# Optimization experiments

Hardware: AMD Instinct MI355X
Metric: run time of the kernel (lower is better)

The kernel has to match this reference:

```python
import jax, jax.numpy as jnp
import numpy as np

N_HEADS = 16


def setup_inputs() -> dict:
    key = jax.random.key(0)
    k1, k2, k3 = jax.random.split(key, 3)
    B, T, D = 2, 2048, 1024
    x = jax.random.normal(k1, (B, T, D), dtype=jnp.float32)
    w_qkv = jax.random.normal(k2, (3 * D, D), dtype=jnp.float32) * 0.02
    w_proj = jax.random.normal(k3, (D, D), dtype=jnp.float32) * (0.02 / np.sqrt(24.0))
    return {"x": x, "w_qkv": w_qkv, "w_proj": w_proj}


def reference(x, w_qkv, w_proj):
    B, T, D = x.shape
    H = N_HEADS
    dh = D // H
    # qkv linear (no bias): x @ w_qkv.T -> [B, T, 3D]
    qkv = jnp.einsum('btd,ed->bte', x, w_qkv)
    q, k, v = jnp.split(qkv, 3, axis=-1)
    q = q.reshape(B, T, H, dh)
    k = k.reshape(B, T, H, dh)
    v = v.reshape(B, T, H, dh)
    # attention with materialized scores [B, H, T, S]
    scores = jnp.einsum('bthd,bshd->bhts', q, k) / jnp.sqrt(jnp.asarray(dh, x.dtype))
    attn = jax.nn.softmax(scores.astype(jnp.float32), axis=-1).astype(x.dtype)
    out = jnp.einsum('bhts,bshd->bthd', attn, v).reshape(B, T, D)
    # output projection (no bias)
    return jnp.einsum('btd,ed->bte', out, w_proj)
```

## Files before the change

kernel.cpp:

```cpp
#include <hip/hip_runtime.h>


typedef __attribute__((ext_vector_type(8))) short s8v;
typedef __attribute__((ext_vector_type(4))) short s4v;
typedef __attribute__((ext_vector_type(8))) unsigned short us8;
typedef __attribute__((ext_vector_type(4))) float f4v;

__device__ __forceinline__ unsigned short f2b(float f) {
    unsigned u = __builtin_bit_cast(unsigned, f);
    u += 0x7FFFu + ((u >> 16) & 1u);
    return (unsigned short)(u >> 16);
}

#if __has_builtin(__builtin_amdgcn_exp2f)
#define EXP2F(x) __builtin_amdgcn_exp2f(x)
#else
#define EXP2F(x) exp2f(x)
#endif

__global__ __launch_bounds__(256) void cvt_all(const float* __restrict__ x,
                                               const float* __restrict__ wq,
                                               const float* __restrict__ wp,
                                               unsigned short* __restrict__ xb,
                                               unsigned short* __restrict__ wqb,
                                               unsigned short* __restrict__ wpb) {
    const int nx = 4096 * 1024 / 4, nq = 3072 * 1024 / 4;
    int i = blockIdx.x * 256 + threadIdx.x;
    const float* s;
    unsigned short* d;
    int j;
    if (i < nx)           { s = x;  d = xb;  j = i; }
    else if (i < nx + nq) { s = wq; d = wqb; j = i - nx; }
    else                  { s = wp; d = wpb; j = i - nx - nq; }
    float4 v = ((const float4*)s)[j];
    ushort4 o;
    o.x = f2b(v.x); o.y = f2b(v.y); o.z = f2b(v.z); o.w = f2b(v.w);
    ((ushort4*)d)[j] = o;
}

#define GLD_LDS16(g, l)                                                                        \
    __builtin_amdgcn_global_load_lds((const __attribute__((address_space(1))) unsigned*)(g),   \
                                     (__attribute__((address_space(3))) unsigned*)(l), 16, 0, 0)

template <bool BF16OUT>
__global__ __launch_bounds__(256) void gemm_nt_bf16(const unsigned short* __restrict__ A,
                                                    const unsigned short* __restrict__ B,
                                                    void* __restrict__ Cv,
                                                    int M, int N, int K) {
    __shared__ unsigned short As[128][32];
    __shared__ unsigned short Bs[128][32];

    const int tid = threadIdx.x;
    const int l = tid & 63, w = tid >> 6;
    const int quad = l >> 4, ln = l & 15;
    const int m0 = blockIdx.y * 128, n0 = blockIdx.x * 128;
    const int wm = (w >> 1) * 64, wn = (w & 1) * 64;

    const f4v fz = {0.f, 0.f, 0.f, 0.f};
    f4v acc[4][4];
#pragma unroll
    for (int i = 0; i < 4; ++i)
#pragma unroll
        for (int j = 0; j < 4; ++j) acc[i][j] = fz;

    const int row0 = tid >> 2, kc = tid & 3;
    for (int k0 = 0; k0 < K; k0 += 32) {
        GLD_LDS16(A + (size_t)(m0 + row0) * K + k0 + kc * 8, &As[row0][kc * 8]);
        GLD_LDS16(B + (size_t)(n0 + row0) * K + k0 + kc * 8, &Bs[row0][kc * 8]);
        GLD_LDS16(A + (size_t)(m0 + row0 + 64) * K + k0 + kc * 8, &As[row0 + 64][kc * 8]);
        GLD_LDS16(B + (size_t)(n0 + row0 + 64) * K + k0 + kc * 8, &Bs[row0 + 64][kc * 8]);
        __syncthreads();

        s8v af[4], bf[4];
#pragma unroll
        for (int mt = 0; mt < 4; ++mt) af[mt] = *(const s8v*)&As[wm + mt * 16 + ln][quad * 8];
#pragma unroll
        for (int nt = 0; nt < 4; ++nt) bf[nt] = *(const s8v*)&Bs[wn + nt * 16 + ln][quad * 8];
#pragma unroll
        for (int mt = 0; mt < 4; ++mt)
#pragma unroll
            for (int nt = 0; nt < 4; ++nt)
                acc[mt][nt] = __builtin_amdgcn_mfma_f32_16x16x32_bf16(af[mt], bf[nt], acc[mt][nt], 0, 0, 0);
        __syncthreads();
    }

#pragma unroll
    for (int mt = 0; mt < 4; ++mt)
#pragma unroll
        for (int nt = 0; nt < 4; ++nt) {
            const size_t row = (size_t)(m0 + wm + mt * 16 + quad * 4);
            const int col = n0 + wn + nt * 16 + ln;
            if (BF16OUT) {
                unsigned short* C = (unsigned short*)Cv;
#pragma unroll
                for (int r = 0; r < 4; ++r) C[(row + r) * N + col] = f2b(acc[mt][nt][r]);
            } else {
                float* C = (float*)Cv;
#pragma unroll
                for (int r = 0; r < 4; ++r) C[(row + r) * N + col] = acc[mt][nt][r];
            }
        }
}

__global__ __launch_bounds__(256) void vtrans(const unsigned short* __restrict__ qkvb,
                                              unsigned short* __restrict__ vtb) {
    __shared__ unsigned Ls[64][65];
    const int tid = threadIdx.x;
    const int t0 = blockIdx.x * 64, h = blockIdx.y, b = blockIdx.z;
#pragma unroll
    for (int it = 0; it < 2; ++it) {
        int idx = tid + it * 256;
        int r = idx >> 3, c8 = idx & 7;
        us8 v = *(const us8*)(qkvb + ((size_t)b * 2048 + t0 + r) * 3072 + 2048 + h * 64 + c8 * 8);
#pragma unroll
        for (int j = 0; j < 8; ++j) Ls[r][c8 * 8 + j] = v[j];
    }
    __syncthreads();
#pragma unroll
    for (int it = 0; it < 2; ++it) {
        int idx = tid + it * 256;
        int d = idx >> 3, tc = idx & 7;
        us8 o;
#pragma unroll
        for (int j = 0; j < 8; ++j) o[j] = (unsigned short)Ls[tc * 8 + j][d];
        *(us8*)(vtb + ((size_t)(b * 16 + h) * 64 + d) * 2048 + t0 + tc * 8) = o;
    }
}

__global__ __launch_bounds__(256) void attn_mfma(const unsigned short* __restrict__ qkvb,
                                                 const unsigned short* __restrict__ vtb,
                                                 unsigned short* __restrict__ attnb) {
    __shared__ unsigned short Qs[64][72];
    __shared__ unsigned short Ks[64][72];
    __shared__ unsigned short Vt[64][72];
    __shared__ unsigned short Ps[64][76];

    const int tid = threadIdx.x;
    const int l = tid & 63, w = tid >> 6;
    const int quad = l >> 4, ln = l & 15;
    const int qb = w * 16;
    const int t0 = blockIdx.x * 64;
    const int h = blockIdx.y, b = blockIdx.z;
    const size_t rowbase = (size_t)b * 2048;
    const unsigned short* Vg = vtb + (size_t)(b * 16 + h) * 64 * 2048;

    const int r0 = tid >> 3,         c0 = (tid & 7) * 8;
    const int r1 = (tid + 256) >> 3, c1 = c0;

    *(us8*)&Qs[r0][c0] = *(const us8*)(qkvb + (rowbase + t0 + r0) * 3072 + h * 64 + c0);
    *(us8*)&Qs[r1][c1] = *(const us8*)(qkvb + (rowbase + t0 + r1) * 3072 + h * 64 + c1);

    const f4v fz = {0.f, 0.f, 0.f, 0.f};
    f4v oacc[4];
#pragma unroll
    for (int i = 0; i < 4; ++i) oacc[i] = fz;
    float lsum[4] = {0.f, 0.f, 0.f, 0.f};

    us8 kreg0 = *(const us8*)(qkvb + (rowbase + r0) * 3072 + 1024 + h * 64 + c0);
    us8 kreg1 = *(const us8*)(qkvb + (rowbase + r1) * 3072 + 1024 + h * 64 + c1);
    us8 vreg0 = *(const us8*)(Vg + (size_t)r0 * 2048 + c0);
    us8 vreg1 = *(const us8*)(Vg + (size_t)r1 * 2048 + c1);

    const float C = 0.18033688011112042f;

    for (int s0 = 0; s0 < 2048; s0 += 64) {
        __syncthreads();
        *(us8*)&Ks[r0][c0] = kreg0;
        *(us8*)&Ks[r1][c1] = kreg1;
        *(us8*)&Vt[r0][c0] = vreg0;
        *(us8*)&Vt[r1][c1] = vreg1;
        __syncthreads();

        if (s0 + 64 < 2048) {
            const int sn = s0 + 64;
            kreg0 = *(const us8*)(qkvb + (rowbase + sn + r0) * 3072 + 1024 + h * 64 + c0);
            kreg1 = *(const us8*)(qkvb + (rowbase + sn + r1) * 3072 + 1024 + h * 64 + c1);
            vreg0 = *(const us8*)(Vg + (size_t)r0 * 2048 + sn + c0);
            vreg1 = *(const us8*)(Vg + (size_t)r1 * 2048 + sn + c1);
        }

        f4v sacc[4];
#pragma unroll
        for (int i = 0; i < 4; ++i) sacc[i] = fz;
#pragma unroll
        for (int ks = 0; ks < 2; ++ks) {
            s8v af = *(const s8v*)&Qs[qb + ln][ks * 32 + quad * 8];
#pragma unroll
            for (int nt = 0; nt < 4; ++nt) {
                s8v bf = *(const s8v*)&Ks[nt * 16 + ln][ks * 32 + quad * 8];
                sacc[nt] = __builtin_amdgcn_mfma_f32_16x16x32_bf16(af, bf, sacc[nt], 0, 0, 0);
            }
        }

#pragma unroll
        for (int nt = 0; nt < 4; ++nt)
#pragma unroll
            for (int r = 0; r < 4; ++r) {
                float p = EXP2F(sacc[nt][r] * C);
                lsum[r] += p;
                Ps[qb + quad * 4 + r][nt * 16 + ln] = f2b(p);
            }

#pragma unroll
        for (int ks = 0; ks < 2; ++ks) {
            s4v plo = *(const s4v*)&Ps[qb + ln][ks * 32 + quad * 8];
            s4v phi = *(const s4v*)&Ps[qb + ln][ks * 32 + quad * 8 + 4];
            s8v pf = __builtin_shufflevector(plo, phi, 0, 1, 2, 3, 4, 5, 6, 7);
#pragma unroll
            for (int nt = 0; nt < 4; ++nt) {
                s8v vf = *(const s8v*)&Vt[nt * 16 + ln][ks * 32 + quad * 8];
                oacc[nt] = __builtin_amdgcn_mfma_f32_16x16x32_bf16(pf, vf, oacc[nt], 0, 0, 0);
            }
        }
    }

    float inv[4];
#pragma unroll
    for (int r = 0; r < 4; ++r) {
        float v = lsum[r];
        v += __shfl_xor(v, 1, 64);
        v += __shfl_xor(v, 2, 64);
        v += __shfl_xor(v, 4, 64);
        v += __shfl_xor(v, 8, 64);
        inv[r] = 1.0f / v;
    }

#pragma unroll
    for (int nt = 0; nt < 4; ++nt)
#pragma unroll
        for (int r = 0; r < 4; ++r) {
            float o = oacc[nt][r] * inv[r];
            attnb[(rowbase + t0 + qb + quad * 4 + r) * 1024 + h * 64 + nt * 16 + ln] = f2b(o);
        }
}

extern "C" void kernel_launch(void* const* d_in, const int* in_sizes, int n_in,
                              void* d_out, int out_size, void* d_ws, size_t ws_size,
                              hipStream_t stream) {
    const float* x      = (const float*)d_in[0];
    const float* w_qkv  = (const float*)d_in[1];
    const float* w_proj = (const float*)d_in[2];
    float* out = (float*)d_out;

    char* p = (char*)d_ws;
    unsigned short* xb    = (unsigned short*)p;  p += (size_t)4096 * 1024 * 2;
    unsigned short* wqb   = (unsigned short*)p;  p += (size_t)3072 * 1024 * 2;
    unsigned short* wpb   = (unsigned short*)p;  p += (size_t)1024 * 1024 * 2;
    unsigned short* qkvb  = (unsigned short*)p;  p += (size_t)4096 * 3072 * 2;
    unsigned short* vtb   = (unsigned short*)p;  p += (size_t)2 * 16 * 64 * 2048 * 2;
    unsigned short* attnb = (unsigned short*)p;  p += (size_t)4096 * 1024 * 2;

    cvt_all<<<8192, 256, 0, stream>>>(x, w_qkv, w_proj, xb, wqb, wpb);

    gemm_nt_bf16<true><<<dim3(3072 / 128, 4096 / 128), 256, 0, stream>>>(xb, wqb, qkvb, 4096, 3072, 1024);

    vtrans<<<dim3(32, 16, 2), 256, 0, stream>>>(qkvb, vtb);

    attn_mfma<<<dim3(32, 16, 2), 256, 0, stream>>>(qkvb, vtb, attnb);

    gemm_nt_bf16<false><<<dim3(1024 / 128, 4096 / 128), 256, 0, stream>>>(attnb, wpb, out, 4096, 1024, 1024);
}
```

Baseline: 215.0 us.

## Fuse V transpose and Q scaling into QKV GEMM, use 32x32 MFMA attention

The QKV GEMM epilogue now writes Q pre-scaled by the softmax constant, writes K into a compact buffer, and writes V already transposed, so the separate vtrans kernel is gone. The attention kernel handles 128 query rows per block with 32x32x16 MFMAs, writes P with packed bf16 stores, and reduces row sums through LDS. The output projection uses a 128x64 tile to launch more blocks for the narrow N=1024 GEMM. Risks are scattered strided stores for the transposed V in the epilogue, higher register and LDS use in attention, and bf16 rounding of the scaled Q.

```diff
diff --git a/kernel.cpp b/kernel.cpp
--- a/kernel.cpp
+++ b/kernel.cpp
@@ -2,14 +2,21 @@
 
 
 typedef __attribute__((ext_vector_type(8))) short s8v;
-typedef __attribute__((ext_vector_type(4))) short s4v;
 typedef __attribute__((ext_vector_type(8))) unsigned short us8;
 typedef __attribute__((ext_vector_type(4))) float f4v;
+typedef __attribute__((ext_vector_type(16))) float f16v;
 
 __device__ __forceinline__ unsigned short f2b(float f) {
     unsigned u = __builtin_bit_cast(unsigned, f);
     u += 0x7FFFu + ((u >> 16) & 1u);
     return (unsigned short)(u >> 16);
+}
+__device__ __forceinline__ unsigned pack2(float a, float b) {
+    unsigned ua = __builtin_bit_cast(unsigned, a);
+    ua += 0x7FFFu + ((ua >> 16) & 1u);
+    unsigned ub = __builtin_bit_cast(unsigned, b);
+    ub += 0x7FFFu + ((ub >> 16) & 1u);
+    return (ua >> 16) | (ub & 0xFFFF0000u);
 }
 
 #if __has_builtin(__builtin_amdgcn_exp2f)
@@ -17,6 +24,8 @@
 #else
 #define EXP2F(x) exp2f(x)
 #endif
+
+#define QSCALE 0.18033688011112042f
 
 __global__ __launch_bounds__(256) void cvt_all(const float* __restrict__ x,
                                                const float* __restrict__ wq,
@@ -42,14 +51,12 @@
     __builtin_amdgcn_global_load_lds((const __attribute__((address_space(1))) unsigned*)(g),   \
                                      (__attribute__((address_space(3))) unsigned*)(l), 16, 0, 0)
 
-template <bool BF16OUT>
-__global__ __launch_bounds__(256) void gemm_nt_bf16(const unsigned short* __restrict__ A,
-                                                    const unsigned short* __restrict__ B,
-                                                    void* __restrict__ Cv,
-                                                    int M, int N, int K) {
+__global__ __launch_bounds__(256) void gemm_qkv(const unsigned short* __restrict__ A,
+                                                const unsigned short* __restrict__ B,
+                                                unsigned short* __restrict__ qkb,
+                                                unsigned short* __restrict__ vtb) {
     __shared__ unsigned short As[128][32];
     __shared__ unsigned short Bs[128][32];
-
     const int tid = threadIdx.x;
     const int l = tid & 63, w = tid >> 6;
     const int quad = l >> 4, ln = l & 15;
@@ -64,13 +71,12 @@
         for (int j = 0; j < 4; ++j) acc[i][j] = fz;
 
     const int row0 = tid >> 2, kc = tid & 3;
-    for (int k0 = 0; k0 < K; k0 += 32) {
-        GLD_LDS16(A + (size_t)(m0 + row0) * K + k0 + kc * 8, &As[row0][kc * 8]);
-        GLD_LDS16(B + (size_t)(n0 + row0) * K + k0 + kc * 8, &Bs[row0][kc * 8]);
-        GLD_LDS16(A + (size_t)(m0 + row0 + 64) * K + k0 + kc * 8, &As[row0 + 64][kc * 8]);
-        GLD_LDS16(B + (size_t)(n0 + row0 + 64) * K + k0 + kc * 8, &Bs[row0 + 64][kc * 8]);
-        __syncthreads();
-
+    for (int k0 = 0; k0 < 1024; k0 += 32) {
+        GLD_LDS16(A + (size_t)(m0 + row0) * 1024 + k0 + kc * 8, &As[row0][kc * 8]);
+        GLD_LDS16(B + (size_t)(n0 + row0) * 1024 + k0 + kc * 8, &Bs[row0][kc * 8]);
+        GLD_LDS16(A + (size_t)(m0 + row0 + 64) * 1024 + k0 + kc * 8, &As[row0 + 64][kc * 8]);
+        GLD_LDS16(B + (size_t)(n0 + row0 + 64) * 1024 + k0 + kc * 8, &Bs[row0 + 64][kc * 8]);
+        __syncthreads();
         s8v af[4], bf[4];
 #pragma unroll
         for (int mt = 0; mt < 4; ++mt) af[mt] = *(const s8v*)&As[wm + mt * 16 + ln][quad * 8];
@@ -88,150 +94,185 @@
     for (int mt = 0; mt < 4; ++mt)
 #pragma unroll
         for (int nt = 0; nt < 4; ++nt) {
-            const size_t row = (size_t)(m0 + wm + mt * 16 + quad * 4);
             const int col = n0 + wn + nt * 16 + ln;
-            if (BF16OUT) {
-                unsigned short* C = (unsigned short*)Cv;
-#pragma unroll
-                for (int r = 0; r < 4; ++r) C[(row + r) * N + col] = f2b(acc[mt][nt][r]);
+            const int row = m0 + wm + mt * 16 + quad * 4;
+            f4v a = acc[mt][nt];
+            if (col < 2048) {
+                const float sc = (col < 1024) ? QSCALE : 1.0f;
+#pragma unroll
+                for (int r = 0; r < 4; ++r)
+                    qkb[(size_t)(row + r) * 2048 + col] = f2b(a[r] * sc);
             } else {
-                float* C = (float*)Cv;
-#pragma unroll
-                for (int r = 0; r < 4; ++r) C[(row + r) * N + col] = acc[mt][nt][r];
-            }
-        }
-}
-
-__global__ __launch_bounds__(256) void vtrans(const unsigned short* __restrict__ qkvb,
-                                              unsigned short* __restrict__ vtb) {
-    __shared__ unsigned Ls[64][65];
-    const int tid = threadIdx.x;
-    const int t0 = blockIdx.x * 64, h = blockIdx.y, b = blockIdx.z;
-#pragma unroll
-    for (int it = 0; it < 2; ++it) {
-        int idx = tid + it * 256;
-        int r = idx >> 3, c8 = idx & 7;
-        us8 v = *(const us8*)(qkvb + ((size_t)b * 2048 + t0 + r) * 3072 + 2048 + h * 64 + c8 * 8);
-#pragma unroll
-        for (int j = 0; j < 8; ++j) Ls[r][c8 * 8 + j] = v[j];
-    }
-    __syncthreads();
-#pragma unroll
-    for (int it = 0; it < 2; ++it) {
-        int idx = tid + it * 256;
-        int d = idx >> 3, tc = idx & 7;
-        us8 o;
-#pragma unroll
-        for (int j = 0; j < 8; ++j) o[j] = (unsigned short)Ls[tc * 8 + j][d];
-        *(us8*)(vtb + ((size_t)(b * 16 + h) * 64 + d) * 2048 + t0 + tc * 8) = o;
-    }
-}
-
-__global__ __launch_bounds__(256) void attn_mfma(const unsigned short* __restrict__ qkvb,
-                                                 const unsigned short* __restrict__ vtb,
-                                                 unsigned short* __restrict__ attnb) {
-    __shared__ unsigned short Qs[64][72];
-    __shared__ unsigned short Ks[64][72];
-    __shared__ unsigned short Vt[64][72];
-    __shared__ unsigned short Ps[64][76];
-
+                const int vd = col - 2048, hh = vd >> 6, dd = vd & 63;
+                const int bb = row >> 11, t = row & 2047;
+                uint2 pk;
+                pk.x = pack2(a[0], a[1]);
+                pk.y = pack2(a[2], a[3]);
+                *(uint2*)&vtb[((size_t)(bb * 16 + hh) * 64 + dd) * 2048 + t] = pk;
+            }
+        }
+}
+
+__global__ __launch_bounds__(256) void gemm_proj(const unsigned short* __restrict__ A,
+                                                 const unsigned short* __restrict__ B,
+                                                 float* __restrict__ C) {
+    __shared__ unsigned short As[128][32];
+    __shared__ unsigned short Bs[64][32];
     const int tid = threadIdx.x;
     const int l = tid & 63, w = tid >> 6;
     const int quad = l >> 4, ln = l & 15;
-    const int qb = w * 16;
-    const int t0 = blockIdx.x * 64;
-    const int h = blockIdx.y, b = blockIdx.z;
-    const size_t rowbase = (size_t)b * 2048;
-    const unsigned short* Vg = vtb + (size_t)(b * 16 + h) * 64 * 2048;
-
-    const int r0 = tid >> 3,         c0 = (tid & 7) * 8;
-    const int r1 = (tid + 256) >> 3, c1 = c0;
-
-    *(us8*)&Qs[r0][c0] = *(const us8*)(qkvb + (rowbase + t0 + r0) * 3072 + h * 64 + c0);
-    *(us8*)&Qs[r1][c1] = *(const us8*)(qkvb + (rowbase + t0 + r1) * 3072 + h * 64 + c1);
+    const int m0 = blockIdx.y * 128, n0 = blockIdx.x * 64;
+    const int wm = w * 32;
 
     const f4v fz = {0.f, 0.f, 0.f, 0.f};
-    f4v oacc[4];
-#pragma unroll
-    for (int i = 0; i < 4; ++i) oacc[i] = fz;
-    float lsum[4] = {0.f, 0.f, 0.f, 0.f};
-
-    us8 kreg0 = *(const us8*)(qkvb + (rowbase + r0) * 3072 + 1024 + h * 64 + c0);
-    us8 kreg1 = *(const us8*)(qkvb + (rowbase + r1) * 3072 + 1024 + h * 64 + c1);
+    f4v acc[2][4];
+#pragma unroll
+    for (int i = 0; i < 2; ++i)
+#pragma unroll
+        for (int j = 0; j < 4; ++j) acc[i][j] = fz;
+
+    const int row0 = tid >> 2, kc = tid & 3;
+    for (int k0 = 0; k0 < 1024; k0 += 32) {
+        GLD_LDS16(A + (size_t)(m0 + row0) * 1024 + k0 + kc * 8, &As[row0][kc * 8]);
+        GLD_LDS16(A + (size_t)(m0 + row0 + 64) * 1024 + k0 + kc * 8, &As[row0 + 64][kc * 8]);
+        GLD_LDS16(B + (size_t)(n0 + row0) * 1024 + k0 + kc * 8, &Bs[row0][kc * 8]);
+        __syncthreads();
+        s8v af[2], bf[4];
+#pragma unroll
+        for (int mt = 0; mt < 2; ++mt) af[mt] = *(const s8v*)&As[wm + mt * 16 + ln][quad * 8];
+#pragma unroll
+        for (int nt = 0; nt < 4; ++nt) bf[nt] = *(const s8v*)&Bs[nt * 16 + ln][quad * 8];
+#pragma unroll
+        for (int mt = 0; mt < 2; ++mt)
+#pragma unroll
+            for (int nt = 0; nt < 4; ++nt)
+                acc[mt][nt] = __builtin_amdgcn_mfma_f32_16x16x32_bf16(af[mt], bf[nt], acc[mt][nt], 0, 0, 0);
+        __syncthreads();
+    }
+
+#pragma unroll
+    for (int mt = 0; mt < 2; ++mt)
+#pragma unroll
+        for (int nt = 0; nt < 4; ++nt) {
+            const int row = m0 + wm + mt * 16 + quad * 4;
+            const int col = n0 + nt * 16 + ln;
+#pragma unroll
+            for (int r = 0; r < 4; ++r) C[(size_t)(row + r) * 1024 + col] = acc[mt][nt][r];
+        }
+}
+
+__global__ __launch_bounds__(256) void attn_mfma(const unsigned short* __restrict__ qkb,
+                                                 const unsigned short* __restrict__ vtb,
+                                                 unsigned short* __restrict__ attnb) {
+    __shared__ unsigned short Qs[128][76];
+    __shared__ unsigned short Ks[64][76];
+    __shared__ unsigned short Vt[64][76];
+    __shared__ unsigned short Ps[128][76];
+    __shared__ float lred[128];
+
+    const int tid = threadIdx.x;
+    const int l = tid & 63, w = tid >> 6;
+    const int m31 = l & 31, h2 = l >> 5;
+    const int qw = w * 32;
+    const int t0 = blockIdx.x * 128;
+    const int hh = blockIdx.y, bb = blockIdx.z;
+    const size_t rowbase = (size_t)bb * 2048;
+    const unsigned short* Vg = vtb + (size_t)(bb * 16 + hh) * 64 * 2048;
+
+#pragma unroll
+    for (int it = 0; it < 4; ++it) {
+        const int idx = tid + it * 256;
+        const int qr = idx >> 3, qc = (idx & 7) * 8;
+        *(us8*)&Qs[qr][qc] = *(const us8*)(qkb + (rowbase + t0 + qr) * 2048 + hh * 64 + qc);
+    }
+
+    const int r0 = tid >> 3, c0 = (tid & 7) * 8;
+
+    f16v zz;
+#pragma unroll
+    for (int i = 0; i < 16; ++i) zz[i] = 0.f;
+    f16v oacc[2];
+    oacc[0] = zz; oacc[1] = zz;
+    float lsum = 0.f;
+
+    us8 kreg0 = *(const us8*)(qkb + (rowbase + r0) * 2048 + 1024 + hh * 64 + c0);
+    us8 kreg1 = *(const us8*)(qkb + (rowbase + r0 + 32) * 2048 + 1024 + hh * 64 + c0);
     us8 vreg0 = *(const us8*)(Vg + (size_t)r0 * 2048 + c0);
-    us8 vreg1 = *(const us8*)(Vg + (size_t)r1 * 2048 + c1);
-
-    const float C = 0.18033688011112042f;
+    us8 vreg1 = *(const us8*)(Vg + (size_t)(r0 + 32) * 2048 + c0);
 
     for (int s0 = 0; s0 < 2048; s0 += 64) {
         __syncthreads();
         *(us8*)&Ks[r0][c0] = kreg0;
-        *(us8*)&Ks[r1][c1] = kreg1;
+        *(us8*)&Ks[r0 + 32][c0] = kreg1;
         *(us8*)&Vt[r0][c0] = vreg0;
-        *(us8*)&Vt[r1][c1] = vreg1;
+        *(us8*)&Vt[r0 + 32][c0] = vreg1;
         __syncthreads();
 
         if (s0 + 64 < 2048) {
             const int sn = s0 + 64;
-            kreg0 = *(const us8*)(qkvb + (rowbase + sn + r0) * 3072 + 1024 + h * 64 + c0);
-            kreg1 = *(const us8*)(qkvb + (rowbase + sn + r1) * 3072 + 1024 + h * 64 + c1);
+            kreg0 = *(const us8*)(qkb + (rowbase + sn + r0) * 2048 + 1024 + hh * 64 + c0);
+            kreg1 = *(const us8*)(qkb + (rowbase + sn + r0 + 32) * 2048 + 1024 + hh * 64 + c0);
             vreg0 = *(const us8*)(Vg + (size_t)r0 * 2048 + sn + c0);
-            vreg1 = *(const us8*)(Vg + (size_t)r1 * 2048 + sn + c1);
-        }
-
-        f4v sacc[4];
-#pragma unroll
-        for (int i = 0; i < 4; ++i) sacc[i] = fz;
-#pragma unroll
-        for (int ks = 0; ks < 2; ++ks) {
-            s8v af = *(const s8v*)&Qs[qb + ln][ks * 32 + quad * 8];
-#pragma unroll
-            for (int nt = 0; nt < 4; ++nt) {
-                s8v bf = *(const s8v*)&Ks[nt * 16 + ln][ks * 32 + quad * 8];
-                sacc[nt] = __builtin_amdgcn_mfma_f32_16x16x32_bf16(af, bf, sacc[nt], 0, 0, 0);
-            }
-        }
-
-#pragma unroll
-        for (int nt = 0; nt < 4; ++nt)
+            vreg1 = *(const us8*)(Vg + (size_t)(r0 + 32) * 2048 + sn + c0);
+        }
+
+        f16v sacc[2];
+        sacc[0] = zz; sacc[1] = zz;
+#pragma unroll
+        for (int k4 = 0; k4 < 4; ++k4) {
+            s8v qf = *(const s8v*)&Qs[qw + m31][k4 * 16 + h2 * 8];
+#pragma unroll
+            for (int st = 0; st < 2; ++st) {
+                s8v kf = *(const s8v*)&Ks[st * 32 + m31][k4 * 16 + h2 * 8];
+                sacc[st] = __builtin_amdgcn_mfma_f32_32x32x16_bf16(kf, qf, sacc[st], 0, 0, 0);
+            }
+        }
+
+#pragma unroll
+        for (int st = 0; st < 2; ++st)
+#pragma unroll
+            for (int g = 0; g < 4; ++g) {
+                float p0 = EXP2F(sacc[st][g * 4 + 0]);
+                float p1 = EXP2F(sacc[st][g * 4 + 1]);
+                float p2 = EXP2F(sacc[st][g * 4 + 2]);
+                float p3 = EXP2F(sacc[st][g * 4 + 3]);
+                lsum += (p0 + p1) + (p2 + p3);
+                uint2 pk;
+                pk.x = pack2(p0, p1);
+                pk.y = pack2(p2, p3);
+                *(uint2*)&Ps[qw + m31][st * 32 + g * 8 + h2 * 4] = pk;
+            }
+
+#pragma unroll
+        for (int k2 = 0; k2 < 4; ++k2) {
+            s8v pf = *(const s8v*)&Ps[qw + m31][k2 * 16 + h2 * 8];
+#pragma unroll
+            for (int nt = 0; nt < 2; ++nt) {
+                s8v vf = *(const s8v*)&Vt[nt * 32 + m31][k2 * 16 + h2 * 8];
+                oacc[nt] = __builtin_amdgcn_mfma_f32_32x32x16_bf16(pf, vf, oacc[nt], 0, 0, 0);
+            }
+        }
+    }
+
+    lsum += __shfl_xor(lsum, 32, 64);
+    lred[qw + m31] = lsum;
+    float inv[16];
+#pragma unroll
+    for (int g = 0; g < 4; ++g)
+#pragma unroll
+        for (int r = 0; r < 4; ++r)
+            inv[g * 4 + r] = 1.0f / lred[qw + 8 * g + 4 * h2 + r];
+
+#pragma unroll
+    for (int nt = 0; nt < 2; ++nt)
+#pragma unroll
+        for (int g = 0; g < 4; ++g)
 #pragma unroll
             for (int r = 0; r < 4; ++r) {
-                float p = EXP2F(sacc[nt][r] * C);
-                lsum[r] += p;
-                Ps[qb + quad * 4 + r][nt * 16 + ln] = f2b(p);
-            }
-
-#pragma unroll
-        for (int ks = 0; ks < 2; ++ks) {
-            s4v plo = *(const s4v*)&Ps[qb + ln][ks * 32 + quad * 8];
-            s4v phi = *(const s4v*)&Ps[qb + ln][ks * 32 + quad * 8 + 4];
-            s8v pf = __builtin_shufflevector(plo, phi, 0, 1, 2, 3, 4, 5, 6, 7);
-#pragma unroll
-            for (int nt = 0; nt < 4; ++nt) {
-                s8v vf = *(const s8v*)&Vt[nt * 16 + ln][ks * 32 + quad * 8];
-                oacc[nt] = __builtin_amdgcn_mfma_f32_16x16x32_bf16(pf, vf, oacc[nt], 0, 0, 0);
-            }
-        }
-    }
-
-    float inv[4];
-#pragma unroll
-    for (int r = 0; r < 4; ++r) {
-        float v = lsum[r];
-        v += __shfl_xor(v, 1, 64);
-        v += __shfl_xor(v, 2, 64);
-        v += __shfl_xor(v, 4, 64);
-        v += __shfl_xor(v, 8, 64);
-        inv[r] = 1.0f / v;
-    }
-
-#pragma unroll
-    for (int nt = 0; nt < 4; ++nt)
-#pragma unroll
-        for (int r = 0; r < 4; ++r) {
-            float o = oacc[nt][r] * inv[r];
-            attnb[(rowbase + t0 + qb + quad * 4 + r) * 1024 + h * 64 + nt * 16 + ln] = f2b(o);
-        }
+                const int qrow = 8 * g + 4 * h2 + r;
+                float o = oacc[nt][g * 4 + r] * inv[g * 4 + r];
+                attnb[(rowbase + t0 + qw + qrow) * 1024 + hh * 64 + nt * 32 + m31] = f2b(o);
+            }
 }
 
 extern "C" void kernel_launch(void* const* d_in, const int* in_sizes, int n_in,
@@ -246,17 +287,15 @@
     unsigned short* xb    = (unsigned short*)p;  p += (size_t)4096 * 1024 * 2;
     unsigned short* wqb   = (unsigned short*)p;  p += (size_t)3072 * 1024 * 2;
     unsigned short* wpb   = (unsigned short*)p;  p += (size_t)1024 * 1024 * 2;
-    unsigned short* qkvb  = (unsigned short*)p;  p += (size_t)4096 * 3072 * 2;
+    unsigned short* qkb   = (unsigned short*)p;  p += (size_t)4096 * 2048 * 2;
     unsigned short* vtb   = (unsigned short*)p;  p += (size_t)2 * 16 * 64 * 2048 * 2;
     unsigned short* attnb = (unsigned short*)p;  p += (size_t)4096 * 1024 * 2;
 
     cvt_all<<<8192, 256, 0, stream>>>(x, w_qkv, w_proj, xb, wqb, wpb);
 
-    gemm_nt_bf16<true><<<dim3(3072 / 128, 4096 / 128), 256, 0, stream>>>(xb, wqb, qkvb, 4096, 3072, 1024);
-
-    vtrans<<<dim3(32, 16, 2), 256, 0, stream>>>(qkvb, vtb);
-
-    attn_mfma<<<dim3(32, 16, 2), 256, 0, stream>>>(qkvb, vtb, attnb);
-
-    gemm_nt_bf16<false><<<dim3(1024 / 128, 4096 / 128), 256, 0, stream>>>(attnb, wpb, out, 4096, 1024, 1024);
-}
+    gemm_qkv<<<dim3(3072 / 128, 4096 / 128), 256, 0, stream>>>(xb, wqb, qkb, vtb);
+
+    attn_mfma<<<dim3(2048 / 128, 16, 2), 256, 0, stream>>>(qkb, vtb, attnb);
+
+    gemm_proj<<<dim3(1024 / 64, 4096 / 128), 256, 0, stream>>>(attnb, wpb, out);
+}
```

New measurement: 209.7 us. 1.03x faster.
